# Kernel optimization log

Hardware: AMD Instinct MI355X
Metric: run time of the kernel (lower is better)

Reference implementation:

```python
import jax, jax.numpy as jnp
import numpy as np

N = 50000      # nodes
E = 800000     # edges
F = 64         # num_features
H = 64         # hidden_channels
L = 3          # num_layers
C0 = 16        # conv1d_channels[0]
TOTAL = H * L + 1  # 193, concat dim / Conv1d kernel size


def setup_inputs() -> dict:
    key = jax.random.key(0)
    ks = jax.random.split(key, 13)
    s = 0.05
    x = jax.random.normal(ks[0], (N, F), jnp.float32)
    edge_index = jax.random.randint(ks[1], (2, E), 0, N)
    edge_attr = jax.random.normal(ks[2], (E, 1), jnp.float32)
    W0 = jax.random.normal(ks[3], (F, H), jnp.float32) * s
    b0 = jnp.zeros((H,), jnp.float32)
    W1 = jax.random.normal(ks[4], (H, H), jnp.float32) * s
    b1 = jnp.zeros((H,), jnp.float32)
    W2 = jax.random.normal(ks[5], (H, H), jnp.float32) * s
    b2 = jnp.zeros((H,), jnp.float32)
    W3 = jax.random.normal(ks[6], (H, 1), jnp.float32) * s
    b3 = jnp.zeros((1,), jnp.float32)
    conv_w = jax.random.normal(ks[7], (C0, TOTAL), jnp.float32) * s  # Conv1d(1,C0,K=TOTAL,stride=TOTAL) weight squeezed
    conv_b = jnp.zeros((C0,), jnp.float32)
    return dict(x=x, edge_index=edge_index, edge_attr=edge_attr,
                W0=W0, b0=b0, W1=W1, b1=b1, W2=W2, b2=b2, W3=W3, b3=b3,
                conv_w=conv_w, conv_b=conv_b)


def _gcn(h, W, b, src, dst, norm):
    # PyG GCNConv: h' = segsum_dst(norm * (h W)[src]) + b
    h = h @ W                                   # [N, out]
    msg = h[src] * norm[:, None]                # [E+N, out] gather (irregular)
    out = jax.ops.segment_sum(msg, dst, num_segments=N)
    return out + b


def reference(x, edge_index, edge_attr, W0, b0, W1, b1, W2, b2, W3, b3, conv_w, conv_b):
    del edge_attr  # use_edge_attr=False
    loops = jnp.arange(N, dtype=edge_index.dtype)
    src = jnp.concatenate([edge_index[0], loops])  # add self-loops
    dst = jnp.concatenate([edge_index[1], loops])
    deg = jax.ops.segment_sum(jnp.ones_like(dst, dtype=x.dtype), dst, num_segments=N)
    dinv = jax.lax.rsqrt(jnp.maximum(deg, 1.0))
    norm = dinv[src] * dinv[dst]

    xs = []
    h = x
    for W, b in ((W0, b0), (W1, b1), (W2, b2), (W3, b3)):
        h = _gcn(h, W, b, src, dst, norm)
        xs.append(h)
    cat = jnp.concatenate(xs, axis=-1)           # [N, TOTAL] (k=1 drops input x)
    # Conv1d(1, C0, K=TOTAL, stride=TOTAL) over length-TOTAL signal == dense projection
    out = cat @ conv_w.T + conv_b                # [N, C0]
    return out
```

## Files before the change

### kernel.cpp

```cpp
#include <hip/hip_runtime.h>
#include <math.h>

static constexpr int N    = 50000;
static constexpr int E    = 800000;
static constexpr int TE   = E + N;
static constexpr int NC   = 16;
static constexpr int TOT  = 193;
static constexpr int NB   = (N + 255) / 256;
static constexpr int DP   = 16;

static constexpr int KQ1 = 0;
static constexpr int KQ2 = 1024;
static constexpr int KQ3 = 2048;
static constexpr int KV  = 3072;
static constexpr int KU1 = 3136;
static constexpr int KU2 = 3152;
static constexpr int KD  = 3168;
static constexpr int KSC = 3184;
static constexpr int KSZ = 3200;

__device__ __forceinline__ unsigned short f2bf(float f) {
    union { float f; unsigned int i; } v; v.f = f;
    unsigned int b = v.i + 0x7FFFu + ((v.i >> 16) & 1u);
    return (unsigned short)(b >> 16);
}


__global__ void k_count(const int* __restrict__ dst, int* __restrict__ degp,
                        int* __restrict__ pos) {
    int e = blockIdx.x * blockDim.x + threadIdx.x;
    if (e < E / 2) {
        int d0 = dst[e], d1 = dst[e + E / 2];
        int p0 = atomicAdd(&degp[d0 * DP], 1);
        int p1 = atomicAdd(&degp[d1 * DP], 1);
        pos[e] = p0;
        pos[e + E / 2] = p1;
    }
}

__global__ __launch_bounds__(256) void k_part(const int* __restrict__ degp,
                                              int* __restrict__ part) {
    __shared__ int red[256];
    const int t = threadIdx.x;
    int i = blockIdx.x * 256 + t;
    int v = (i < N) ? (degp[i * DP] + 1) : 0;
    red[t] = v;
    __syncthreads();
#pragma unroll
    for (int off = 128; off; off >>= 1) {
        if (t < off) red[t] += red[t + off];
        __syncthreads();
    }
    if (t == 0) part[blockIdx.x] = red[0];
}

__global__ __launch_bounds__(256) void k_scanpart(int* __restrict__ part) {
    __shared__ int s[256];
    const int t = threadIdx.x;
    int v = (t < NB) ? part[t] : 0;
    s[t] = v;
    __syncthreads();
#pragma unroll
    for (int off = 1; off < 256; off <<= 1) {
        int u = (t >= off) ? s[t - off] : 0;
        __syncthreads();
        s[t] += u;
        __syncthreads();
    }
    if (t < NB) part[t] = s[t] - v;
}

__global__ __launch_bounds__(256) void k_scatter(const int* __restrict__ degp,
                                                 const int* __restrict__ part,
                                                 int* __restrict__ row_ptr,
                                                 float* __restrict__ dinv) {
    __shared__ int s[256];
    const int t = threadIdx.x;
    int i = blockIdx.x * 256 + t;
    int v = (i < N) ? (degp[i * DP] + 1) : 0;
    s[t] = v;
    __syncthreads();
#pragma unroll
    for (int off = 1; off < 256; off <<= 1) {
        int u = (t >= off) ? s[t - off] : 0;
        __syncthreads();
        s[t] += u;
        __syncthreads();
    }
    if (i < N) {
        int base = part[blockIdx.x];
        row_ptr[i] = base + s[t] - v;
        dinv[i] = rsqrtf((float)v);
        if (i == N - 1) row_ptr[N] = base + s[t];
    }
}

__global__ void k_fill(const int* __restrict__ src, const int* __restrict__ dst,
                       const int* __restrict__ pos,
                       const int* __restrict__ row_ptr,
                       const float* __restrict__ dinv,
                       int2* __restrict__ edges) {
    int idx = blockIdx.x * blockDim.x + threadIdx.x;
    if (idx < E) {
        int s = src[idx], d = dst[idx];
        int p = row_ptr[d] + 1 + pos[idx];
        edges[p] = make_int2(s, __float_as_int(dinv[s] * dinv[d]));
    } else if (idx < TE) {
        int i = idx - E;
        float dv = dinv[i];
        edges[row_ptr[i]] = make_int2(i, __float_as_int(dv * dv));
    }
}

__global__ __launch_bounds__(256) void k_xbf(const float* __restrict__ x,
                                             ushort* __restrict__ xb) {
    int i = blockIdx.x * 256 + threadIdx.x;
    if (i * 4 >= N * 64) return;
    float4 v = ((const float4*)x)[i];
    ushort4 o;
    o.x = f2bf(v.x); o.y = f2bf(v.y); o.z = f2bf(v.z); o.w = f2bf(v.w);
    ((ushort4*)xb)[i] = o;
}

__global__ __launch_bounds__(256) void k_setup(
    const float* __restrict__ W0, const float* __restrict__ b0,
    const float* __restrict__ W1, const float* __restrict__ b1,
    const float* __restrict__ W2, const float* __restrict__ b2,
    const float* __restrict__ W3, const float* __restrict__ b3,
    const float* __restrict__ cw, const float* __restrict__ cb,
    float* __restrict__ K) {
    __shared__ float W0s[4096], W1s[4096], W2s[4096], P2s[4096];
    __shared__ float C1[1024], C2[1024], C3[1024], R3s[1024];
    __shared__ float W3s[64], b0s[64], b1s[64], b2s[64];
    __shared__ float r3[64], rb1[64], rb2[64], rb12[64];
    const int t = threadIdx.x;
    const int k = t >> 2, q = t & 3;

    for (int i = t; i < 4096; i += 256) {
        W0s[i] = W0[i]; W1s[i] = W1[i]; W2s[i] = W2[i];
    }
    for (int i = t; i < 1024; i += 256) {
        int j = i >> 4, c = i & 15;
        C1[i] = cw[c * TOT + j];
        C2[i] = cw[c * TOT + 64 + j];
        C3[i] = cw[c * TOT + 128 + j];
    }
    if (t < 64) { W3s[t] = W3[t]; b0s[t] = b0[t]; b1s[t] = b1[t]; b2s[t] = b2[t]; }
    __syncthreads();

    {
        const int j0 = q * 16;
        float acc[16];
#pragma unroll
        for (int jj = 0; jj < 16; ++jj) acc[jj] = 0.f;
        for (int m = 0; m < 64; ++m) {
            float w = W0s[k * 64 + m];
#pragma unroll
            for (int jj = 0; jj < 16; ++jj) acc[jj] += w * W1s[m * 64 + j0 + jj];
        }
#pragma unroll
        for (int jj = 0; jj < 16; ++jj) P2s[k * 64 + j0 + jj] = acc[jj];
    }
    {
        const int c0 = q * 4;
        float acc[4] = {0.f, 0.f, 0.f, 0.f};
        for (int j = 0; j < 64; ++j) {
            float w = W2s[k * 64 + j];
#pragma unroll
            for (int cc = 0; cc < 4; ++cc) acc[cc] += w * C3[j * 16 + c0 + cc];
        }
#pragma unroll
        for (int cc = 0; cc < 4; ++cc) R3s[k * 16 + c0 + cc] = acc[cc];
    }
    if (q == 0) {
        float a = 0.f;
        for (int j = 0; j < 64; ++j) a += W2s[k * 64 + j] * W3s[j];
        r3[k] = a;
    }
    if (q == 1) {
        float a = 0.f;
        for (int m = 0; m < 64; ++m) a += b0s[m] * W1s[m * 64 + k];
        rb1[k] = a;
    }
    if (q == 2) {
        float a = 0.f;
        for (int m = 0; m < 64; ++m) a += b1s[m] * W2s[m * 64 + k];
        rb2[k] = a;
    }
    __syncthreads();

    {
        const int c0 = q * 4;
        float q1[4] = {0,0,0,0}, q2[4] = {0,0,0,0}, q3[4] = {0,0,0,0};
        for (int j = 0; j < 64; ++j) {
            float w0 = W0s[k * 64 + j], p2 = P2s[k * 64 + j];
#pragma unroll
            for (int cc = 0; cc < 4; ++cc) {
                q1[cc] += w0 * C1[j * 16 + c0 + cc];
                q2[cc] += p2 * C2[j * 16 + c0 + cc];
                q3[cc] += p2 * R3s[j * 16 + c0 + cc];
            }
        }
#pragma unroll
        for (int cc = 0; cc < 4; ++cc) {
            K[KQ1 + k * 16 + c0 + cc] = q1[cc];
            K[KQ2 + k * 16 + c0 + cc] = q2[cc];
            K[KQ3 + k * 16 + c0 + cc] = q3[cc];
        }
    }
    if (q == 3) {
        float a = 0.f;
        for (int j = 0; j < 64; ++j) a += P2s[k * 64 + j] * r3[j];
        K[KV + k] = a;
    }
    if (q == 0) {
        float a = 0.f;
        for (int m = 0; m < 64; ++m) a += rb1[m] * W2s[m * 64 + k];
        rb12[k] = a;
    }
    __syncthreads();

    if (t < 16) {
        float a1 = 0.f, a2 = 0.f, ad = 0.f;
        for (int j = 0; j < 64; ++j) {
            a1 += rb1[j] * C2[j * 16 + t] + rb2[j] * C3[j * 16 + t];
            a2 += rb12[j] * C3[j * 16 + t];
            ad += b0s[j] * C1[j * 16 + t] + b1s[j] * C2[j * 16 + t]
                + b2s[j] * C3[j * 16 + t];
        }
        K[KU1 + t] = a1; K[KU2 + t] = a2; K[KD + t] = ad + cb[t];
    }
    if (t == 0) {
        float al = 0.f, be = 0.f, ga = 0.f;
        for (int j = 0; j < 64; ++j) {
            al += rb12[j] * W3s[j]; be += rb2[j] * W3s[j]; ga += b2s[j] * W3s[j];
        }
        K[KSC + 0] = al; K[KSC + 1] = be; K[KSC + 2] = ga;
    }
}

template <int LAYER>
__global__ __launch_bounds__(256) void k_layer(
    const ushort* __restrict__ Min,
    const int2* __restrict__ edges,
    const int* __restrict__ row_ptr,
    const float* __restrict__ K,
    const float* __restrict__ s1in,
    const float* __restrict__ s2in,
    ushort* __restrict__ Mout,
    float* __restrict__ s_out,
    float* __restrict__ t4,
    float* __restrict__ out) {
    __shared__ float QT[64 * 17];
    const int tid = threadIdx.x;
    constexpr int KQ = (LAYER == 0) ? KQ1 : (LAYER == 1) ? KQ2 : KQ3;
    for (int i = tid; i < 1024; i += 256) {
        int j = i >> 4, c = i & 15;
        QT[j * 17 + c] = K[KQ + i];
    }
    const int lane = tid & 63;
    const int w    = tid >> 6;
    const int q    = lane >> 4;
    const int m    = lane & 15;
    float v0 = 0.f, v1 = 0.f, v2 = 0.f, v3 = 0.f;
    if constexpr (LAYER == 2) {
        v0 = K[KV + 4 * m + 0]; v1 = K[KV + 4 * m + 1];
        v2 = K[KV + 4 * m + 2]; v3 = K[KV + 4 * m + 3];
    }
    __syncthreads();

    const int nn = blockIdx.x * 16 + w * 4 + q;
    const int rp0 = row_ptr[nn], rp1 = row_ptr[nn + 1];
    const int d = rp1 - rp0;
    int dmax = max(d, __shfl_xor(d, 16));
    dmax = max(dmax, __shfl_xor(dmax, 32));
    const int trips = __builtin_amdgcn_readfirstlane((dmax + 7) >> 3);

    float a0 = 0.f, a1 = 0.f, a2 = 0.f, a3 = 0.f, accs = 0.f;
    for (int t = 0; t < trips; ++t) {
        const int base = rp0 + t * 8;
        int col[8]; float wv[8];
#pragma unroll
        for (int i = 0; i < 8; ++i) {
            int pi = base + i;
            int pc = min(pi, rp1 - 1);
            int2 e = edges[pc];
            col[i] = e.x;
            wv[i] = (pi < rp1) ? __int_as_float(e.y) : 0.f;
        }
        unsigned long long g[8];
#pragma unroll
        for (int i = 0; i < 8; ++i)
            g[i] = *(const unsigned long long*)(Min + col[i] * 64 + 4 * m);
        if constexpr (LAYER == 0) {
#pragma unroll
            for (int i = 0; i < 8; ++i) accs += wv[i];
        }
#pragma unroll
        for (int i = 0; i < 8; ++i) {
            unsigned int lo = (unsigned int)g[i];
            unsigned int hi = (unsigned int)(g[i] >> 32);
            union { unsigned int u; float f; } x0, x1, x2, x3;
            x0.u = lo << 16; x1.u = lo & 0xFFFF0000u;
            x2.u = hi << 16; x3.u = hi & 0xFFFF0000u;
            a0 += wv[i] * x0.f; a1 += wv[i] * x1.f;
            a2 += wv[i] * x2.f; a3 += wv[i] * x3.f;
        }
    }

    if constexpr (LAYER < 2) {
        unsigned long long pk =
              (unsigned long long)f2bf(a0)
            | ((unsigned long long)f2bf(a1) << 16)
            | ((unsigned long long)f2bf(a2) << 32)
            | ((unsigned long long)f2bf(a3) << 48);
        ((unsigned long long*)Mout)[nn * 16 + m] = pk;
    }
    if constexpr (LAYER == 0) {
        if (m == 0) s_out[nn] = accs;
    }
    if constexpr (LAYER == 1) {
        float ss = 0.f;
        for (int p = rp0 + m; p < rp1; p += 16) {
            int2 e = edges[p];
            ss += __int_as_float(e.y) * s1in[e.x];
        }
        ss += __shfl_xor(ss, 1); ss += __shfl_xor(ss, 2);
        ss += __shfl_xor(ss, 4); ss += __shfl_xor(ss, 8);
        if (m == 0) s_out[nn] = ss;
    }

    float s1n = 0.f, s2n = 0.f;
    if constexpr (LAYER == 2) {
        s1n = s1in[nn]; s2n = s2in[nn];
        float tv = a0 * v0 + a1 * v1 + a2 * v2 + a3 * v3;
        tv += __shfl_xor(tv, 1); tv += __shfl_xor(tv, 2);
        tv += __shfl_xor(tv, 4); tv += __shfl_xor(tv, 8);
        if (m == 0)
            t4[nn] = tv + K[KSC + 0] * s2n + K[KSC + 1] * s1n + K[KSC + 2];
    }

    float r = 0.f;
#pragma unroll
    for (int a = 0; a < 16; ++a) {
        int srcl = (q << 4) + a;
        float f0 = __shfl(a0, srcl), f1 = __shfl(a1, srcl);
        float f2 = __shfl(a2, srcl), f3 = __shfl(a3, srcl);
        r += f0 * QT[(4 * a + 0) * 17 + m] + f1 * QT[(4 * a + 1) * 17 + m]
           + f2 * QT[(4 * a + 2) * 17 + m] + f3 * QT[(4 * a + 3) * 17 + m];
    }
    {
        int o = nn * NC + m;
        if constexpr (LAYER == 0) {
            out[o] = K[KD + m] + r;
        } else if constexpr (LAYER == 1) {
            out[o] += r;
        } else {
            out[o] += r + s1n * K[KU1 + m] + s2n * K[KU2 + m];
        }
    }
}

__global__ __launch_bounds__(256) void k_agg4_out(
    const float* __restrict__ t4, const int2* __restrict__ edges,
    const int* __restrict__ row_ptr, const float* __restrict__ b3,
    const float* __restrict__ conv_w, float* __restrict__ out) {
    int n = blockIdx.x * blockDim.x + threadIdx.x;
    if (n >= N) return;
    int p0 = row_ptr[n], p1 = row_ptr[n + 1];
    float a0 = 0.f, a1 = 0.f;
    for (int p = p0; p < p1; p += 4) {
        int q0 = min(p, p1 - 1), q1 = min(p + 1, p1 - 1);
        int q2 = min(p + 2, p1 - 1), q3 = min(p + 3, p1 - 1);
        int2 e0 = edges[q0], e1 = edges[q1], e2 = edges[q2], e3 = edges[q3];
        float w0 = __int_as_float(e0.y);
        float w1 = (p + 1 < p1) ? __int_as_float(e1.y) : 0.f;
        float w2 = (p + 2 < p1) ? __int_as_float(e2.y) : 0.f;
        float w3 = (p + 3 < p1) ? __int_as_float(e3.y) : 0.f;
        a0 += w0 * t4[e0.x]; a1 += w1 * t4[e1.x];
        a0 += w2 * t4[e2.x]; a1 += w3 * t4[e3.x];
    }
    float h4 = a0 + a1 + b3[0];
    float4* o4 = (float4*)(out + n * NC);
#pragma unroll
    for (int k = 0; k < 4; ++k) {
        float4 v = o4[k];
        v.x += h4 * conv_w[(4 * k + 0) * TOT + 192];
        v.y += h4 * conv_w[(4 * k + 1) * TOT + 192];
        v.z += h4 * conv_w[(4 * k + 2) * TOT + 192];
        v.w += h4 * conv_w[(4 * k + 3) * TOT + 192];
        o4[k] = v;
    }
}


extern "C" void kernel_launch(void* const* d_in, const int* in_sizes, int n_in,
                              void* d_out, int out_size, void* d_ws, size_t ws_size,
                              hipStream_t stream) {
    const float* x   = (const float*)d_in[0];
    const int*   ei  = (const int*)d_in[1];
    const int*   src = ei;
    const int*   dst = ei + E;
    const float* W0  = (const float*)d_in[3];
    const float* b0  = (const float*)d_in[4];
    const float* W1  = (const float*)d_in[5];
    const float* b1  = (const float*)d_in[6];
    const float* W2  = (const float*)d_in[7];
    const float* b2  = (const float*)d_in[8];
    const float* W3  = (const float*)d_in[9];
    const float* b3  = (const float*)d_in[10];
    const float* cw  = (const float*)d_in[11];
    const float* cb  = (const float*)d_in[12];
    float* out = (float*)d_out;

    char* p = (char*)d_ws;
    auto alloc = [&](size_t nbytes) {
        char* r = p;
        p += (nbytes + 255) & ~(size_t)255;
        return (void*)r;
    };
    int*    degp    = (int*)alloc((size_t)N * DP * 4);
    int*    pos     = (int*)alloc((size_t)E * 4);
    int*    row_ptr = (int*)alloc((size_t)(N + 1) * 4);
    float*  dinv    = (float*)alloc((size_t)N * 4);
    int*    part    = (int*)alloc((size_t)NB * 4);
    int2*   edges   = (int2*)alloc((size_t)TE * 8);
    ushort* xb      = (ushort*)alloc((size_t)N * 64 * 2);
    ushort* M1      = (ushort*)alloc((size_t)N * 64 * 2);
    ushort* M2      = (ushort*)alloc((size_t)N * 64 * 2);
    float*  s1      = (float*)alloc((size_t)N * 4);
    float*  s2      = (float*)alloc((size_t)N * 4);
    float*  t4      = (float*)alloc((size_t)N * 4);
    float*  K       = (float*)alloc((size_t)KSZ * 4);

    k_setup<<<1, 256, 0, stream>>>(W0, b0, W1, b1, W2, b2, W3, b3, cw, cb, K);
    k_xbf<<<(N * 64 / 4 + 255) / 256, 256, 0, stream>>>(x, xb);

    hipMemsetAsync(degp, 0, (size_t)N * DP * 4, stream);
    k_count   <<<(E / 2 + 255) / 256, 256, 0, stream>>>(dst, degp, pos);
    k_part    <<<NB, 256, 0, stream>>>(degp, part);
    k_scanpart<<<1, 256, 0, stream>>>(part);
    k_scatter <<<NB, 256, 0, stream>>>(degp, part, row_ptr, dinv);
    k_fill    <<<(TE + 255) / 256, 256, 0, stream>>>(src, dst, pos, row_ptr, dinv, edges);

    const int layerGrid = N / 16;

    k_layer<0><<<layerGrid, 256, 0, stream>>>(
        xb, edges, row_ptr, K, nullptr, nullptr, M1, s1, nullptr, out);
    k_layer<1><<<layerGrid, 256, 0, stream>>>(
        M1, edges, row_ptr, K, s1, nullptr, M2, s2, nullptr, out);
    k_layer<2><<<layerGrid, 256, 0, stream>>>(
        M2, edges, row_ptr, K, s1, s2, nullptr, nullptr, t4, out);
    k_agg4_out<<<(N + 255) / 256, 256, 0, stream>>>(t4, edges, row_ptr, b3, cw, out);
}
```

Before: 177.9 us.

## Fuse setup, bf16 conversion and degree memset; prefetch edges in layer loops

Merges the weight-folding setup kernel, the x-to-bf16 conversion and the degree-buffer memset into one launch. The xbf blocks zero degp and the last block does the setup. k_count now handles 8 edges per thread instead of 2, so more atomics are in flight per thread. The layer aggregation loop software-pipelines the edge-list loads, fetching the next 8 (col, weight) pairs while the current gathers are consumed. This is meant to cut launch overhead and hide edge-load latency. The cost is that every fused block reserves the setup kernel's large static LDS, which may limit occupancy of the conversion blocks, and the extra prefetch raises register pressure.

Result: slower. 185.5 us (+4.3%).

```diff
diff --git a/kernel.cpp b/kernel.cpp
--- a/kernel.cpp
+++ b/kernel.cpp
@@ -8,6 +8,7 @@
 static constexpr int TOT  = 193;
 static constexpr int NB   = (N + 255) / 256;
 static constexpr int DP   = 16;
+static constexpr int XBF_BLOCKS = (N * 64 / 4) / 256;
 
 static constexpr int KQ1 = 0;
 static constexpr int KQ2 = 1024;
@@ -25,16 +26,146 @@
     return (unsigned short)(b >> 16);
 }
 
+__global__ __launch_bounds__(256) void k_setup_xbf(
+    const float* __restrict__ x, ushort* __restrict__ xb, int* __restrict__ degp,
+    const float* __restrict__ W0, const float* __restrict__ b0,
+    const float* __restrict__ W1, const float* __restrict__ b1,
+    const float* __restrict__ W2, const float* __restrict__ b2,
+    const float* __restrict__ W3, const float* __restrict__ b3,
+    const float* __restrict__ cw, const float* __restrict__ cb,
+    float* __restrict__ K) {
+    const int t = threadIdx.x;
+    if (blockIdx.x < XBF_BLOCKS) {
+        int i = blockIdx.x * 256 + t;
+        degp[i] = 0;
+        float4 v = ((const float4*)x)[i];
+        ushort4 o;
+        o.x = f2bf(v.x); o.y = f2bf(v.y); o.z = f2bf(v.z); o.w = f2bf(v.w);
+        ((ushort4*)xb)[i] = o;
+        return;
+    }
+    __shared__ float W0s[4096], W1s[4096], W2s[4096], P2s[4096];
+    __shared__ float C1[1024], C2[1024], C3[1024], R3s[1024];
+    __shared__ float W3s[64], b0s[64], b1s[64], b2s[64];
+    __shared__ float r3[64], rb1[64], rb2[64], rb12[64];
+    const int k = t >> 2, q = t & 3;
+
+    for (int i = t; i < 4096; i += 256) {
+        W0s[i] = W0[i]; W1s[i] = W1[i]; W2s[i] = W2[i];
+    }
+    for (int i = t; i < 1024; i += 256) {
+        int j = i >> 4, c = i & 15;
+        C1[i] = cw[c * TOT + j];
+        C2[i] = cw[c * TOT + 64 + j];
+        C3[i] = cw[c * TOT + 128 + j];
+    }
+    if (t < 64) { W3s[t] = W3[t]; b0s[t] = b0[t]; b1s[t] = b1[t]; b2s[t] = b2[t]; }
+    __syncthreads();
+
+    {
+        const int j0 = q * 16;
+        float acc[16];
+#pragma unroll
+        for (int jj = 0; jj < 16; ++jj) acc[jj] = 0.f;
+        for (int m = 0; m < 64; ++m) {
+            float w = W0s[k * 64 + m];
+#pragma unroll
+            for (int jj = 0; jj < 16; ++jj) acc[jj] += w * W1s[m * 64 + j0 + jj];
+        }
+#pragma unroll
+        for (int jj = 0; jj < 16; ++jj) P2s[k * 64 + j0 + jj] = acc[jj];
+    }
+    {
+        const int c0 = q * 4;
+        float acc[4] = {0.f, 0.f, 0.f, 0.f};
+        for (int j = 0; j < 64; ++j) {
+            float w = W2s[k * 64 + j];
+#pragma unroll
+            for (int cc = 0; cc < 4; ++cc) acc[cc] += w * C3[j * 16 + c0 + cc];
+        }
+#pragma unroll
+        for (int cc = 0; cc < 4; ++cc) R3s[k * 16 + c0 + cc] = acc[cc];
+    }
+    if (q == 0) {
+        float a = 0.f;
+        for (int j = 0; j < 64; ++j) a += W2s[k * 64 + j] * W3s[j];
+        r3[k] = a;
+    }
+    if (q == 1) {
+        float a = 0.f;
+        for (int m = 0; m < 64; ++m) a += b0s[m] * W1s[m * 64 + k];
+        rb1[k] = a;
+    }
+    if (q == 2) {
+        float a = 0.f;
+        for (int m = 0; m < 64; ++m) a += b1s[m] * W2s[m * 64 + k];
+        rb2[k] = a;
+    }
+    __syncthreads();
+
+    {
+        const int c0 = q * 4;
+        float q1[4] = {0,0,0,0}, q2[4] = {0,0,0,0}, q3[4] = {0,0,0,0};
+        for (int j = 0; j < 64; ++j) {
+            float w0 = W0s[k * 64 + j], p2 = P2s[k * 64 + j];
+#pragma unroll
+            for (int cc = 0; cc < 4; ++cc) {
+                q1[cc] += w0 * C1[j * 16 + c0 + cc];
+                q2[cc] += p2 * C2[j * 16 + c0 + cc];
+                q3[cc] += p2 * R3s[j * 16 + c0 + cc];
+            }
+        }
+#pragma unroll
+        for (int cc = 0; cc < 4; ++cc) {
+            K[KQ1 + k * 16 + c0 + cc] = q1[cc];
+            K[KQ2 + k * 16 + c0 + cc] = q2[cc];
+            K[KQ3 + k * 16 + c0 + cc] = q3[cc];
+        }
+    }
+    if (q == 3) {
+        float a = 0.f;
+        for (int j = 0; j < 64; ++j) a += P2s[k * 64 + j] * r3[j];
+        K[KV + k] = a;
+    }
+    if (q == 0) {
+        float a = 0.f;
+        for (int m = 0; m < 64; ++m) a += rb1[m] * W2s[m * 64 + k];
+        rb12[k] = a;
+    }
+    __syncthreads();
+
+    if (t < 16) {
+        float a1 = 0.f, a2 = 0.f, ad = 0.f;
+        for (int j = 0; j < 64; ++j) {
+            a1 += rb1[j] * C2[j * 16 + t] + rb2[j] * C3[j * 16 + t];
+            a2 += rb12[j] * C3[j * 16 + t];
+            ad += b0s[j] * C1[j * 16 + t] + b1s[j] * C2[j * 16 + t]
+                + b2s[j] * C3[j * 16 + t];
+        }
+        K[KU1 + t] = a1; K[KU2 + t] = a2; K[KD + t] = ad + cb[t];
+    }
+    if (t == 0) {
+        float al = 0.f, be = 0.f, ga = 0.f;
+        for (int j = 0; j < 64; ++j) {
+            al += rb12[j] * W3s[j]; be += rb2[j] * W3s[j]; ga += b2s[j] * W3s[j];
+        }
+        K[KSC + 0] = al; K[KSC + 1] = be; K[KSC + 2] = ga;
+    }
+}
 
 __global__ void k_count(const int* __restrict__ dst, int* __restrict__ degp,
                         int* __restrict__ pos) {
+    const int S = E / 8;
     int e = blockIdx.x * blockDim.x + threadIdx.x;
-    if (e < E / 2) {
-        int d0 = dst[e], d1 = dst[e + E / 2];
-        int p0 = atomicAdd(&degp[d0 * DP], 1);
-        int p1 = atomicAdd(&degp[d1 * DP], 1);
-        pos[e] = p0;
-        pos[e + E / 2] = p1;
+    if (e < S) {
+        int d[8];
+#pragma unroll
+        for (int k = 0; k < 8; ++k) d[k] = dst[e + k * S];
+        int p[8];
+#pragma unroll
+        for (int k = 0; k < 8; ++k) p[k] = atomicAdd(&degp[d[k] * DP], 1);
+#pragma unroll
+        for (int k = 0; k < 8; ++k) pos[e + k * S] = p[k];
     }
 }
 
@@ -109,133 +240,6 @@
         int i = idx - E;
         float dv = dinv[i];
         edges[row_ptr[i]] = make_int2(i, __float_as_int(dv * dv));
-    }
-}
-
-__global__ __launch_bounds__(256) void k_xbf(const float* __restrict__ x,
-                                             ushort* __restrict__ xb) {
-    int i = blockIdx.x * 256 + threadIdx.x;
-    if (i * 4 >= N * 64) return;
-    float4 v = ((const float4*)x)[i];
-    ushort4 o;
-    o.x = f2bf(v.x); o.y = f2bf(v.y); o.z = f2bf(v.z); o.w = f2bf(v.w);
-    ((ushort4*)xb)[i] = o;
-}
-
-__global__ __launch_bounds__(256) void k_setup(
-    const float* __restrict__ W0, const float* __restrict__ b0,
-    const float* __restrict__ W1, const float* __restrict__ b1,
-    const float* __restrict__ W2, const float* __restrict__ b2,
-    const float* __restrict__ W3, const float* __restrict__ b3,
-    const float* __restrict__ cw, const float* __restrict__ cb,
-    float* __restrict__ K) {
-    __shared__ float W0s[4096], W1s[4096], W2s[4096], P2s[4096];
-    __shared__ float C1[1024], C2[1024], C3[1024], R3s[1024];
-    __shared__ float W3s[64], b0s[64], b1s[64], b2s[64];
-    __shared__ float r3[64], rb1[64], rb2[64], rb12[64];
-    const int t = threadIdx.x;
-    const int k = t >> 2, q = t & 3;
-
-    for (int i = t; i < 4096; i += 256) {
-        W0s[i] = W0[i]; W1s[i] = W1[i]; W2s[i] = W2[i];
-    }
-    for (int i = t; i < 1024; i += 256) {
-        int j = i >> 4, c = i & 15;
-        C1[i] = cw[c * TOT + j];
-        C2[i] = cw[c * TOT + 64 + j];
-        C3[i] = cw[c * TOT + 128 + j];
-    }
-    if (t < 64) { W3s[t] = W3[t]; b0s[t] = b0[t]; b1s[t] = b1[t]; b2s[t] = b2[t]; }
-    __syncthreads();
-
-    {
-        const int j0 = q * 16;
-        float acc[16];
-#pragma unroll
-        for (int jj = 0; jj < 16; ++jj) acc[jj] = 0.f;
-        for (int m = 0; m < 64; ++m) {
-            float w = W0s[k * 64 + m];
-#pragma unroll
-            for (int jj = 0; jj < 16; ++jj) acc[jj] += w * W1s[m * 64 + j0 + jj];
-        }
-#pragma unroll
-        for (int jj = 0; jj < 16; ++jj) P2s[k * 64 + j0 + jj] = acc[jj];
-    }
-    {
-        const int c0 = q * 4;
-        float acc[4] = {0.f, 0.f, 0.f, 0.f};
-        for (int j = 0; j < 64; ++j) {
-            float w = W2s[k * 64 + j];
-#pragma unroll
-            for (int cc = 0; cc < 4; ++cc) acc[cc] += w * C3[j * 16 + c0 + cc];
-        }
-#pragma unroll
-        for (int cc = 0; cc < 4; ++cc) R3s[k * 16 + c0 + cc] = acc[cc];
-    }
-    if (q == 0) {
-        float a = 0.f;
-        for (int j = 0; j < 64; ++j) a += W2s[k * 64 + j] * W3s[j];
-        r3[k] = a;
-    }
-    if (q == 1) {
-        float a = 0.f;
-        for (int m = 0; m < 64; ++m) a += b0s[m] * W1s[m * 64 + k];
-        rb1[k] = a;
-    }
-    if (q == 2) {
-        float a = 0.f;
-        for (int m = 0; m < 64; ++m) a += b1s[m] * W2s[m * 64 + k];
-        rb2[k] = a;
-    }
-    __syncthreads();
-
-    {
-        const int c0 = q * 4;
-        float q1[4] = {0,0,0,0}, q2[4] = {0,0,0,0}, q3[4] = {0,0,0,0};
-        for (int j = 0; j < 64; ++j) {
-            float w0 = W0s[k * 64 + j], p2 = P2s[k * 64 + j];
-#pragma unroll
-            for (int cc = 0; cc < 4; ++cc) {
-                q1[cc] += w0 * C1[j * 16 + c0 + cc];
-                q2[cc] += p2 * C2[j * 16 + c0 + cc];
-                q3[cc] += p2 * R3s[j * 16 + c0 + cc];
-            }
-        }
-#pragma unroll
-        for (int cc = 0; cc < 4; ++cc) {
-            K[KQ1 + k * 16 + c0 + cc] = q1[cc];
-            K[KQ2 + k * 16 + c0 + cc] = q2[cc];
-            K[KQ3 + k * 16 + c0 + cc] = q3[cc];
-        }
-    }
-    if (q == 3) {
-        float a = 0.f;
-        for (int j = 0; j < 64; ++j) a += P2s[k * 64 + j] * r3[j];
-        K[KV + k] = a;
-    }
-    if (q == 0) {
-        float a = 0.f;
-        for (int m = 0; m < 64; ++m) a += rb1[m] * W2s[m * 64 + k];
-        rb12[k] = a;
-    }
-    __syncthreads();
-
-    if (t < 16) {
-        float a1 = 0.f, a2 = 0.f, ad = 0.f;
-        for (int j = 0; j < 64; ++j) {
-            a1 += rb1[j] * C2[j * 16 + t] + rb2[j] * C3[j * 16 + t];
-            a2 += rb12[j] * C3[j * 16 + t];
-            ad += b0s[j] * C1[j * 16 + t] + b1s[j] * C2[j * 16 + t]
-                + b2s[j] * C3[j * 16 + t];
-        }
-        K[KU1 + t] = a1; K[KU2 + t] = a2; K[KD + t] = ad + cb[t];
-    }
-    if (t == 0) {
-        float al = 0.f, be = 0.f, ga = 0.f;
-        for (int j = 0; j < 64; ++j) {
-            al += rb12[j] * W3s[j]; be += rb2[j] * W3s[j]; ga += b2s[j] * W3s[j];
-        }
-        K[KSC + 0] = al; K[KSC + 1] = be; K[KSC + 2] = ga;
     }
 }
 
@@ -277,21 +281,30 @@
     const int trips = __builtin_amdgcn_readfirstlane((dmax + 7) >> 3);
 
     float a0 = 0.f, a1 = 0.f, a2 = 0.f, a3 = 0.f, accs = 0.f;
+    int col[8]; float wv[8];
+#pragma unroll
+    for (int i = 0; i < 8; ++i) {
+        int pi = rp0 + i;
+        int pc = min(pi, rp1 - 1);
+        int2 e = edges[pc];
+        col[i] = e.x;
+        wv[i] = (pi < rp1) ? __int_as_float(e.y) : 0.f;
+    }
     for (int t = 0; t < trips; ++t) {
-        const int base = rp0 + t * 8;
-        int col[8]; float wv[8];
+        unsigned long long g[8];
+#pragma unroll
+        for (int i = 0; i < 8; ++i)
+            g[i] = *(const unsigned long long*)(Min + col[i] * 64 + 4 * m);
+        const int nb = rp0 + (t + 1) * 8;
+        int ncol[8]; float nwv[8];
 #pragma unroll
         for (int i = 0; i < 8; ++i) {
-            int pi = base + i;
+            int pi = nb + i;
             int pc = min(pi, rp1 - 1);
             int2 e = edges[pc];
-            col[i] = e.x;
-            wv[i] = (pi < rp1) ? __int_as_float(e.y) : 0.f;
-        }
-        unsigned long long g[8];
-#pragma unroll
-        for (int i = 0; i < 8; ++i)
-            g[i] = *(const unsigned long long*)(Min + col[i] * 64 + 4 * m);
+            ncol[i] = e.x;
+            nwv[i] = (pi < rp1) ? __int_as_float(e.y) : 0.f;
+        }
         if constexpr (LAYER == 0) {
 #pragma unroll
             for (int i = 0; i < 8; ++i) accs += wv[i];
@@ -306,6 +319,8 @@
             a0 += wv[i] * x0.f; a1 += wv[i] * x1.f;
             a2 += wv[i] * x2.f; a3 += wv[i] * x3.f;
         }
+#pragma unroll
+        for (int i = 0; i < 8; ++i) { col[i] = ncol[i]; wv[i] = nwv[i]; }
     }
 
     if constexpr (LAYER < 2) {
@@ -433,11 +448,10 @@
     float*  t4      = (float*)alloc((size_t)N * 4);
     float*  K       = (float*)alloc((size_t)KSZ * 4);
 
-    k_setup<<<1, 256, 0, stream>>>(W0, b0, W1, b1, W2, b2, W3, b3, cw, cb, K);
-    k_xbf<<<(N * 64 / 4 + 255) / 256, 256, 0, stream>>>(x, xb);
-
-    hipMemsetAsync(degp, 0, (size_t)N * DP * 4, stream);
-    k_count   <<<(E / 2 + 255) / 256, 256, 0, stream>>>(dst, degp, pos);
+    k_setup_xbf<<<XBF_BLOCKS + 1, 256, 0, stream>>>(
+        x, xb, degp, W0, b0, W1, b1, W2, b2, W3, b3, cw, cb, K);
+
+    k_count   <<<(E / 8 + 255) / 256, 256, 0, stream>>>(dst, degp, pos);
     k_part    <<<NB, 256, 0, stream>>>(degp, part);
     k_scanpart<<<1, 256, 0, stream>>>(part);
     k_scatter <<<NB, 256, 0, stream>>>(degp, part, row_ptr, dinv);
```
